# Kernel optimization log

Measured on AMD Instinct MI355X. Metric: run time of the kernel, lower is better.

## Reference

```python
import jax, jax.numpy as jnp
import numpy as np

N = 100000   # nodes
E = 1600000  # directed edges (before self loops)
IN = 64
HID = 32     # per-head hidden channels
H = 4        # heads
OUT = 32     # final output channels
NEG_SLOPE = 0.2
LN_EPS = 1e-5


def setup_inputs() -> dict:
    key = jax.random.key(0)
    ks = jax.random.split(key, 24)
    def nrm(k, shape, s=0.1):
        return jax.random.normal(k, shape, jnp.float32) * s
    inp = {
        "x": jax.random.normal(ks[0], (N, IN), jnp.float32),
        "edge_index": jax.random.randint(ks[1], (2, E), 0, N, jnp.int32),
    }
    in_dims = [IN, H * HID, H * HID]
    j = 2
    for i, di in enumerate(in_dims):
        inp[f"W{i}"] = nrm(ks[j], (di, H * HID)); j += 1
        inp[f"as{i}"] = nrm(ks[j], (H, HID)); j += 1
        inp[f"ad{i}"] = nrm(ks[j], (H, HID)); j += 1
        inp[f"b{i}"] = jnp.zeros((H * HID,), jnp.float32)
        inp[f"g{i}"] = jnp.ones((H * HID,), jnp.float32)
        inp[f"be{i}"] = jnp.zeros((H * HID,), jnp.float32)
    inp["Wf"] = nrm(ks[j], (H * HID, OUT)); j += 1
    inp["asf"] = nrm(ks[j], (1, OUT)); j += 1
    inp["adf"] = nrm(ks[j], (1, OUT)); j += 1
    inp["bf"] = jnp.zeros((OUT,), jnp.float32)
    return inp


def gat_conv(x, src, dst, W, att_s, att_d, bias, heads, C, concat, n_nodes):
    # h: [N, H, C]
    h = (x @ W).reshape(n_nodes, heads, C)
    a_src = jnp.sum(h * att_s, axis=-1)  # [N, H]
    a_dst = jnp.sum(h * att_d, axis=-1)  # [N, H]
    e = jax.nn.leaky_relu(a_src[src] + a_dst[dst], NEG_SLOPE)  # [E', H]
    # segment softmax over incoming edges of each dst node
    m = jax.ops.segment_max(e, dst, num_segments=n_nodes)
    m = jnp.where(jnp.isfinite(m), m, 0.0)
    ex = jnp.exp(e - m[dst])
    denom = jax.ops.segment_sum(ex, dst, num_segments=n_nodes)
    alpha = ex / (denom[dst] + 1e-16)  # [E', H]
    msg = h[src] * alpha[..., None]    # [E', H, C]
    out = jax.ops.segment_sum(msg, dst, num_segments=n_nodes)  # [N, H, C]
    if concat:
        out = out.reshape(n_nodes, heads * C)
    else:
        out = out.mean(axis=1)
    return out + bias


def layer_norm(x, g, b):
    mu = x.mean(-1, keepdims=True)
    v = jnp.mean((x - mu) ** 2, axis=-1, keepdims=True)
    return g * (x - mu) / jnp.sqrt(v + LN_EPS) + b


def reference(x, edge_index,
              W0, as0, ad0, b0, g0, be0,
              W1, as1, ad1, b1, g1, be1,
              W2, as2, ad2, b2, g2, be2,
              Wf, asf, adf, bf):
    n_nodes = x.shape[0]
    loop = jnp.arange(n_nodes, dtype=edge_index.dtype)
    src = jnp.concatenate([edge_index[0], loop])  # add self loops (PyG default)
    dst = jnp.concatenate([edge_index[1], loop])
    blocks = [(W0, as0, ad0, b0, g0, be0),
              (W1, as1, ad1, b1, g1, be1),
              (W2, as2, ad2, b2, g2, be2)]
    for (W, a_s, a_d, b, g, be) in blocks:
        x = gat_conv(x, src, dst, W, a_s, a_d, b, H, HID, True, n_nodes)
        x = jax.nn.elu(layer_norm(x, g, be))
    return gat_conv(x, src, dst, Wf, asf, adf, bf, 1, OUT, False, n_nodes)
```

## Files before the change

kernel.cpp:

```cpp
#include <hip/hip_runtime.h>
#include <hip/hip_bf16.h>

constexpr int NN   = 100000;
constexpr int EE   = 1600000;
constexpr int ETOT = EE + NN;
constexpr float SLOPE = 0.2f;
constexpr int BSH = 8;
constexpr int NB  = (NN + (1 << BSH) - 1) >> BSH;
constexpr int CCH = 8192;
constexpr int DCAP  = 36;
constexpr int DCAPP = 37;

typedef __attribute__((ext_vector_type(8))) short short8;
typedef __attribute__((ext_vector_type(4))) float f32x4;

__device__ __forceinline__ float bf_lo(unsigned u) { return __uint_as_float(u << 16); }
__device__ __forceinline__ float bf_hi(unsigned u) { return __uint_as_float(u & 0xffff0000u); }
__device__ __forceinline__ unsigned short f2bf(float f) {
    __hip_bfloat16 h = __float2bfloat16(f);
    return *(unsigned short*)&h;
}
__device__ __forceinline__ void wave_lds_fence() {
    __asm__ volatile("s_waitcnt lgkmcnt(0)" ::: "memory");
}
__device__ __forceinline__ void fma8(float* acc, uint4 u, float al) {
    acc[0] += bf_lo(u.x) * al; acc[1] += bf_hi(u.x) * al;
    acc[2] += bf_lo(u.y) * al; acc[3] += bf_hi(u.y) * al;
    acc[4] += bf_lo(u.z) * al; acc[5] += bf_hi(u.z) * al;
    acc[6] += bf_lo(u.w) * al; acc[7] += bf_hi(u.w) * al;
}
__device__ __forceinline__ void fma4(float* acc, uint2 u, float al) {
    acc[0] += bf_lo(u.x) * al; acc[1] += bf_hi(u.x) * al;
    acc[2] += bf_lo(u.y) * al; acc[3] += bf_hi(u.y) * al;
}

__global__ void k_cvt_x(const float* __restrict__ x, unsigned short* __restrict__ xb) {
    int i = blockIdx.x * blockDim.x + threadIdx.x;
    if (i >= NN * 64 / 8) return;
    const float4* xp = (const float4*)(x + (size_t)i * 8);
    float4 v0 = xp[0], v1 = xp[1];
    unsigned short o[8] = {f2bf(v0.x), f2bf(v0.y), f2bf(v0.z), f2bf(v0.w),
                           f2bf(v1.x), f2bf(v1.y), f2bf(v1.z), f2bf(v1.w)};
    *(uint4*)(xb + (size_t)i * 8) = *(uint4*)o;
}

__global__ __launch_bounds__(256) void k_cvt_w_all(
    const float* __restrict__ W0, const float* __restrict__ W1,
    const float* __restrict__ W2, const float* __restrict__ Wf,
    unsigned short* __restrict__ Wt0, unsigned short* __restrict__ Wt1,
    unsigned short* __restrict__ Wt2, unsigned short* __restrict__ Wtf,
    int* __restrict__ gbh) {
    int i = blockIdx.x * 256 + threadIdx.x;
    if (i < NB) gbh[i] = 0;
    if (i < 8192) {
        int k = i / 128, n = i % 128;
        Wt0[n * 64 + k] = f2bf(W0[i]);
    } else if (i < 24576) {
        int j = i - 8192; int k = j / 128, n = j % 128;
        Wt1[n * 128 + k] = f2bf(W1[j]);
    } else if (i < 40960) {
        int j = i - 24576; int k = j / 128, n = j % 128;
        Wt2[n * 128 + k] = f2bf(W2[j]);
    } else if (i < 45056) {
        int j = i - 40960; int k = j / 32, n = j % 32;
        Wtf[n * 128 + k] = f2bf(Wf[j]);
    }
}

__global__ __launch_bounds__(256) void k_bhist(const int* __restrict__ ei,
                                               int* __restrict__ gbh) {
    __shared__ int h[NB];
    int t = threadIdx.x;
    for (int i = t; i < NB; i += 256) h[i] = 0;
    __syncthreads();
    int i = blockIdx.x * 2048 + t;
#pragma unroll
    for (int k = 0; k < 8; k++, i += 256)
        if (i < EE) atomicAdd(&h[ei[EE + i] >> BSH], 1);
    __syncthreads();
    for (int j = t; j < NB; j += 256)
        if (h[j]) atomicAdd(&gbh[j], h[j]);
}

__global__ void k_bscan(const int* __restrict__ gbh, int* __restrict__ ebase,
                        int* __restrict__ gcur) {
    __shared__ int sd[512];
    int t = threadIdx.x;
    int v = (t < NB) ? gbh[t] : 0;
    sd[t] = v;
    __syncthreads();
    for (int off = 1; off < 512; off <<= 1) {
        int x = (t >= off) ? sd[t - off] : 0;
        __syncthreads();
        sd[t] += x;
        __syncthreads();
    }
    int ex = sd[t] - v;
    if (t < NB) { ebase[t] = ex; gcur[t] = ex; }
    if (t == NB) ebase[NB] = EE;
}

__global__ __launch_bounds__(256) void k_bscatter(const int* __restrict__ ei,
                                                  int* __restrict__ gcur,
                                                  int* __restrict__ pbuf) {
    __shared__ int h[NB], base[NB], cur[NB];
    int t = threadIdx.x;
    for (int i = t; i < NB; i += 256) { h[i] = 0; cur[i] = 0; }
    __syncthreads();
    int c0 = blockIdx.x * CCH;
    int cend = c0 + CCH < EE ? c0 + CCH : EE;
    for (int i = c0 + t; i < cend; i += 256)
        atomicAdd(&h[ei[EE + i] >> BSH], 1);
    __syncthreads();
    for (int i = t; i < NB; i += 256)
        if (h[i] > 0) base[i] = atomicAdd(&gcur[i], h[i]);
    __syncthreads();
    for (int i = c0 + t; i < cend; i += 256) {
        int s = ei[i], d = ei[EE + i];
        int b = d >> BSH;
        int c = atomicAdd(&cur[b], 1);
        pbuf[base[b] + c] = s | ((d & ((1 << BSH) - 1)) << 17);
    }
}

__global__ __launch_bounds__(256) void k_bcsr(const int* __restrict__ pbuf,
                                              const int* __restrict__ ebase,
                                              int* __restrict__ row_ptr,
                                              int* __restrict__ esrc) {
    constexpr int BNODES = 1 << BSH;
    __shared__ int hist[BNODES];
    __shared__ int cur[BNODES];
    __shared__ int sd[256];
    int b = blockIdx.x, t = threadIdx.x;
    int node0 = b << BSH;
    int e0 = ebase[b], e1 = ebase[b + 1];
    hist[t] = 0; cur[t] = 0;
    __syncthreads();
    for (int i = e0 + t; i < e1; i += 256)
        atomicAdd(&hist[pbuf[i] >> 17], 1);
    __syncthreads();
    int ts = hist[t];
    sd[t] = ts;
    __syncthreads();
    for (int off = 1; off < 256; off <<= 1) {
        int x = (t >= off) ? sd[t - off] : 0;
        __syncthreads();
        sd[t] += x;
        __syncthreads();
    }
    int ex = sd[t] - ts;
    __syncthreads();
    hist[t] = ex;
    __syncthreads();
    int rbase = e0 + node0;
    int n = node0 + t;
    if (n < NN) {
        int rp = rbase + hist[t] + t;
        row_ptr[n] = rp;
        esrc[rp] = n;
    }
    __syncthreads();
    for (int i = e0 + t; i < e1; i += 256) {
        int p = pbuf[i];
        int nl = p >> 17;
        int c = atomicAdd(&cur[nl], 1);
        esrc[rbase + hist[nl] + nl + 1 + c] = p & 0x1FFFF;
    }
}

template <int BN, int H>
__global__ __launch_bounds__(256) void k_mfma_att(
    const unsigned short* __restrict__ Ab, const unsigned short* __restrict__ Bt,
    const float* __restrict__ as_, const float* __restrict__ ad_,
    unsigned short* __restrict__ hb, float* __restrict__ a_s,
    float* __restrict__ a_d, int M, int K) {
    constexpr int NCT = BN / 16;
    constexpr int LDKB = 136;
    __shared__ unsigned short Bs[BN * LDKB];
    int tid = threadIdx.x;
    int lane = tid & 63, w = tid >> 6;
    int q = lane >> 4, col = lane & 15;
    int rowBase = blockIdx.x * 128;

    int kvs = (K == 64) ? 3 : 4;
    for (int idx = tid; idx < (BN << kvs); idx += 256) {
        int br = idx >> kvs;
        int ko = (idx & ((1 << kvs) - 1)) << 3;
        *(uint4*)(&Bs[br * LDKB + ko]) = *(const uint4*)(Bt + (size_t)br * K + ko);
    }
    __syncthreads();

    f32x4 acc[2][NCT];
#pragma unroll
    for (int rt = 0; rt < 2; rt++)
#pragma unroll
        for (int ct = 0; ct < NCT; ct++) acc[rt][ct] = (f32x4){0.f, 0.f, 0.f, 0.f};

    int r0 = rowBase + w * 32 + col;
    int grc0 = min(r0, M - 1);
    int grc1 = min(r0 + 16, M - 1);
    const unsigned short* a0p = Ab + (size_t)grc0 * K + q * 8;
    const unsigned short* a1p = Ab + (size_t)grc1 * K + q * 8;

    int nph = K >> 6;
    for (int ph = 0; ph < nph; ph++) {
        int kof = ph * 64;
        short8 af[2][2];
        af[0][0] = *(const short8*)(a0p + kof);
        af[0][1] = *(const short8*)(a0p + kof + 32);
        af[1][0] = *(const short8*)(a1p + kof);
        af[1][1] = *(const short8*)(a1p + kof + 32);
#pragma unroll
        for (int kt = 0; kt < 2; kt++)
#pragma unroll
            for (int ct = 0; ct < NCT; ct++) {
                short8 bf = *(const short8*)(&Bs[(ct * 16 + col) * LDKB + kof + kt * 32 + q * 8]);
#pragma unroll
                for (int rt = 0; rt < 2; rt++)
                    acc[rt][ct] = __builtin_amdgcn_mfma_f32_16x16x32_bf16(
                        af[rt][kt], bf, acc[rt][ct], 0, 0, 0);
            }
    }

    float swv[NCT], dwv[NCT];
#pragma unroll
    for (int ct = 0; ct < NCT; ct++) {
        int c = ct * 16 + col;
        swv[ct] = as_[c];
        dwv[ct] = ad_[c];
    }
#pragma unroll
    for (int rt = 0; rt < 2; rt++) {
#pragma unroll
        for (int r = 0; r < 4; r++) {
            int gr = rowBase + w * 32 + rt * 16 + q * 4 + r;
            if constexpr (H == 4) {
                float ps[4] = {0, 0, 0, 0}, pd[4] = {0, 0, 0, 0};
#pragma unroll
                for (int ct = 0; ct < NCT; ct++) {
                    float v = acc[rt][ct][r];
                    ps[ct >> 1] += v * swv[ct];
                    pd[ct >> 1] += v * dwv[ct];
                }
#pragma unroll
                for (int m = 1; m < 16; m <<= 1)
#pragma unroll
                    for (int h = 0; h < 4; h++) {
                        ps[h] += __shfl_xor(ps[h], m);
                        pd[h] += __shfl_xor(pd[h], m);
                    }
                if (gr < M) {
#pragma unroll
                    for (int ct = 0; ct < NCT; ct++)
                        hb[(size_t)gr * BN + ct * 16 + col] = f2bf(acc[rt][ct][r]);
                    if (col == 0) {
                        *(float4*)(a_s + (size_t)gr * 4) = make_float4(ps[0], ps[1], ps[2], ps[3]);
                        *(float4*)(a_d + (size_t)gr * 4) = make_float4(pd[0], pd[1], pd[2], pd[3]);
                    }
                }
            } else {
                float ps = 0.f, pd = 0.f;
#pragma unroll
                for (int ct = 0; ct < NCT; ct++) {
                    float v = acc[rt][ct][r];
                    ps += v * swv[ct];
                    pd += v * dwv[ct];
                }
#pragma unroll
                for (int m = 1; m < 16; m <<= 1) {
                    ps += __shfl_xor(ps, m);
                    pd += __shfl_xor(pd, m);
                }
                if (gr < M) {
#pragma unroll
                    for (int ct = 0; ct < NCT; ct++)
                        hb[(size_t)gr * BN + ct * 16 + col] = f2bf(acc[rt][ct][r]);
                    if (col == 0) { a_s[gr] = ps; a_d[gr] = pd; }
                }
            }
        }
    }
}

__global__ __launch_bounds__(128) void k_aggregate_ln(
    const unsigned short* __restrict__ hb, const float* __restrict__ a_src,
    const float* __restrict__ a_dst, const int* __restrict__ row_ptr,
    const int* __restrict__ esrc, const float* __restrict__ bias,
    const float* __restrict__ gamma, const float* __restrict__ beta,
    unsigned short* __restrict__ xb) {
    __shared__ uint2 slab_all[2][4 * 4 * DCAPP];
    int tid = threadIdx.x;
    int w = tid >> 6, lane = tid & 63;
    int g = lane >> 4, i = lane & 15;
    int myhead = i >> 2;
    uint2* slab = slab_all[w];
    int n0 = blockIdx.x * 8 + w * 4;
    int n = n0 + g;
    bool valid = n < NN;
    int start = 0, deg = 0;
    if (valid) {
        start = row_ptr[n];
        int end = (n == NN - 1) ? ETOT : row_ptr[n + 1];
        deg = end - start;
    }
    int wmax = deg;
#pragma unroll
    for (int m = 1; m < 64; m <<= 1) wmax = max(wmax, __shfl_xor(wmax, m));

    if (wmax <= DCAP) {
        float4 ad = make_float4(0.f, 0.f, 0.f, 0.f);
        if (valid) ad = ((const float4*)a_dst)[n];
        float d0 = 0.f, d1 = 0.f, d2 = 0.f, d3 = 0.f;
        uint2* nslab = slab + g * (4 * DCAPP);
        for (int k = i; k < deg; k += 16) {
            int s = esrc[start + k];
            float4 a = ((const float4*)a_src)[s];
            float e0 = a.x + ad.x; e0 = fmaxf(e0, SLOPE * e0); float x0 = __expf(e0);
            float e1 = a.y + ad.y; e1 = fmaxf(e1, SLOPE * e1); float x1 = __expf(e1);
            float e2 = a.z + ad.z; e2 = fmaxf(e2, SLOPE * e2); float x2 = __expf(e2);
            float e3 = a.w + ad.w; e3 = fmaxf(e3, SLOPE * e3); float x3 = __expf(e3);
            nslab[0 * DCAPP + k] = make_uint2((unsigned)s, __float_as_uint(x0));
            nslab[1 * DCAPP + k] = make_uint2((unsigned)s, __float_as_uint(x1));
            nslab[2 * DCAPP + k] = make_uint2((unsigned)s, __float_as_uint(x2));
            nslab[3 * DCAPP + k] = make_uint2((unsigned)s, __float_as_uint(x3));
            d0 += x0; d1 += x1; d2 += x2; d3 += x3;
        }
#pragma unroll
        for (int m = 1; m < 16; m <<= 1) {
            d0 += __shfl_xor(d0, m);
            d1 += __shfl_xor(d1, m);
            d2 += __shfl_xor(d2, m);
            d3 += __shfl_xor(d3, m);
        }
        float dh = myhead == 0 ? d0 : myhead == 1 ? d1 : myhead == 2 ? d2 : d3;
        float inv = 1.f / (dh + 1e-16f);
        wave_lds_fence();

        float acc[8];
#pragma unroll
        for (int k = 0; k < 8; k++) acc[k] = 0.f;
        const uint2* myrow = nslab + myhead * DCAPP;
        const unsigned short* hbase = hb + i * 8;
        int j = 0;
        for (; j + 4 <= deg; j += 4) {
            uint2 p0 = myrow[j], p1 = myrow[j + 1], p2 = myrow[j + 2], p3 = myrow[j + 3];
            uint4 u0 = *(const uint4*)(hbase + (size_t)p0.x * 128);
            uint4 u1 = *(const uint4*)(hbase + (size_t)p1.x * 128);
            uint4 u2 = *(const uint4*)(hbase + (size_t)p2.x * 128);
            uint4 u3 = *(const uint4*)(hbase + (size_t)p3.x * 128);
            fma8(acc, u0, __uint_as_float(p0.y));
            fma8(acc, u1, __uint_as_float(p1.y));
            fma8(acc, u2, __uint_as_float(p2.y));
            fma8(acc, u3, __uint_as_float(p3.y));
        }
        for (; j < deg; j++) {
            uint2 p = myrow[j];
            uint4 uu = *(const uint4*)(hbase + (size_t)p.x * 128);
            fma8(acc, uu, __uint_as_float(p.y));
        }
#pragma unroll
        for (int k = 0; k < 8; k++) acc[k] *= inv;

        if (valid) {
            float y[8];
            float sum = 0.f;
            const float4* bp = (const float4*)(bias + i * 8);
            float4 b0 = bp[0], b1 = bp[1];
#pragma unroll
            for (int k = 0; k < 8; k++) {
                float b = k < 4 ? (&b0.x)[k] : (&b1.x)[k - 4];
                y[k] = acc[k] + b;
                sum += y[k];
            }
#pragma unroll
            for (int m = 1; m < 16; m <<= 1) sum += __shfl_xor(sum, m);
            float mu = sum * (1.f / 128.f);
            float ss = 0.f;
            float d[8];
#pragma unroll
            for (int k = 0; k < 8; k++) { d[k] = y[k] - mu; ss += d[k] * d[k]; }
#pragma unroll
            for (int m = 1; m < 16; m <<= 1) ss += __shfl_xor(ss, m);
            float is = rsqrtf(ss * (1.f / 128.f) + 1e-5f);
            const float4* gp = (const float4*)(gamma + i * 8);
            const float4* ep = (const float4*)(beta + i * 8);
            float4 g0 = gp[0], g1 = gp[1], e0 = ep[0], e1 = ep[1];
            unsigned short o16[8];
#pragma unroll
            for (int k = 0; k < 8; k++) {
                float gm = k < 4 ? (&g0.x)[k] : (&g1.x)[k - 4];
                float bt = k < 4 ? (&e0.x)[k] : (&e1.x)[k - 4];
                float z = gm * (d[k] * is) + bt;
                o16[k] = f2bf(z > 0.f ? z : __expf(z) - 1.f);
            }
            *(uint4*)(xb + (size_t)n * 128 + i * 8) = *(uint4*)o16;
        }
    } else {
        for (int m4 = 0; m4 < 4; m4++) {
            int nm = n0 + m4;
            if (nm >= NN) continue;
            int startm = row_ptr[nm];
            int endm = (nm == NN - 1) ? ETOT : row_ptr[nm + 1];
            int degm = endm - startm;
            float4 ad = ((const float4*)a_dst)[nm];
            int gg = lane >> 4, c16 = lane & 15, hh = c16 >> 2;
            float acc[8];
#pragma unroll
            for (int k = 0; k < 8; k++) acc[k] = 0.f;
            if (degm <= 64) {
                int msrc = 0;
                float me0 = 0.f, me1 = 0.f, me2 = 0.f, me3 = 0.f;
                if (lane < degm) {
                    int s = esrc[startm + lane];
                    msrc = s;
                    float4 a = ((const float4*)a_src)[s];
                    float e0 = a.x + ad.x; e0 = fmaxf(e0, SLOPE * e0); me0 = __expf(e0);
                    float e1 = a.y + ad.y; e1 = fmaxf(e1, SLOPE * e1); me1 = __expf(e1);
                    float e2 = a.z + ad.z; e2 = fmaxf(e2, SLOPE * e2); me2 = __expf(e2);
                    float e3 = a.w + ad.w; e3 = fmaxf(e3, SLOPE * e3); me3 = __expf(e3);
                }
                float d0 = me0, d1 = me1, d2 = me2, d3 = me3;
#pragma unroll
                for (int m = 1; m < 64; m <<= 1) {
                    d0 += __shfl_xor(d0, m);
                    d1 += __shfl_xor(d1, m);
                    d2 += __shfl_xor(d2, m);
                    d3 += __shfl_xor(d3, m);
                }
                me0 *= 1.f / (d0 + 1e-16f);
                me1 *= 1.f / (d1 + 1e-16f);
                me2 *= 1.f / (d2 + 1e-16f);
                me3 *= 1.f / (d3 + 1e-16f);
                int iters = (degm + 3) >> 2;
                for (int it = 0; it < iters; it++) {
                    int j = gg + (it << 2);
                    int jj = j < degm ? j : 0;
                    int s = __shfl(msrc, jj);
                    float a0 = __shfl(me0, jj), a1 = __shfl(me1, jj);
                    float a2 = __shfl(me2, jj), a3 = __shfl(me3, jj);
                    if (j < degm) {
                        float al = hh == 0 ? a0 : hh == 1 ? a1 : hh == 2 ? a2 : a3;
                        uint4 uu = *(const uint4*)(hb + (size_t)s * 128 + c16 * 8);
                        fma8(acc, uu, al);
                    }
                }
            } else {
                float d0 = 0.f, d1 = 0.f, d2 = 0.f, d3 = 0.f;
                for (int k = startm + lane; k < endm; k += 64) {
                    int s = esrc[k];
                    float4 a = ((const float4*)a_src)[s];
                    float e0 = a.x + ad.x; e0 = fmaxf(e0, SLOPE * e0); d0 += __expf(e0);
                    float e1 = a.y + ad.y; e1 = fmaxf(e1, SLOPE * e1); d1 += __expf(e1);
                    float e2 = a.z + ad.z; e2 = fmaxf(e2, SLOPE * e2); d2 += __expf(e2);
                    float e3 = a.w + ad.w; e3 = fmaxf(e3, SLOPE * e3); d3 += __expf(e3);
                }
#pragma unroll
                for (int m = 1; m < 64; m <<= 1) {
                    d0 += __shfl_xor(d0, m);
                    d1 += __shfl_xor(d1, m);
                    d2 += __shfl_xor(d2, m);
                    d3 += __shfl_xor(d3, m);
                }
                float invh = hh == 0 ? 1.f / (d0 + 1e-16f) : hh == 1 ? 1.f / (d1 + 1e-16f)
                           : hh == 2 ? 1.f / (d2 + 1e-16f) : 1.f / (d3 + 1e-16f);
                float adh = hh == 0 ? ad.x : hh == 1 ? ad.y : hh == 2 ? ad.z : ad.w;
                for (int j = gg; j < degm; j += 4) {
                    int s = esrc[startm + j];
                    float e = a_src[(size_t)s * 4 + hh] + adh;
                    e = fmaxf(e, SLOPE * e);
                    float al = __expf(e) * invh;
                    uint4 uu = *(const uint4*)(hb + (size_t)s * 128 + c16 * 8);
                    fma8(acc, uu, al);
                }
            }
#pragma unroll
            for (int k = 0; k < 8; k++) {
                acc[k] += __shfl_xor(acc[k], 16);
                acc[k] += __shfl_xor(acc[k], 32);
            }
            if (lane < 16) {
                float y[8];
                float sum = 0.f;
                const float4* bp = (const float4*)(bias + lane * 8);
                float4 b0 = bp[0], b1 = bp[1];
#pragma unroll
                for (int k = 0; k < 8; k++) {
                    float b = k < 4 ? (&b0.x)[k] : (&b1.x)[k - 4];
                    y[k] = acc[k] + b;
                    sum += y[k];
                }
#pragma unroll
                for (int m = 1; m < 16; m <<= 1) sum += __shfl_xor(sum, m);
                float mu = sum * (1.f / 128.f);
                float ss = 0.f;
                float d[8];
#pragma unroll
                for (int k = 0; k < 8; k++) { d[k] = y[k] - mu; ss += d[k] * d[k]; }
#pragma unroll
                for (int m = 1; m < 16; m <<= 1) ss += __shfl_xor(ss, m);
                float is = rsqrtf(ss * (1.f / 128.f) + 1e-5f);
                const float4* gp = (const float4*)(gamma + lane * 8);
                const float4* ep = (const float4*)(beta + lane * 8);
                float4 g0 = gp[0], g1 = gp[1], e0 = ep[0], e1 = ep[1];
                unsigned short o16[8];
#pragma unroll
                for (int k = 0; k < 8; k++) {
                    float gm = k < 4 ? (&g0.x)[k] : (&g1.x)[k - 4];
                    float bt = k < 4 ? (&e0.x)[k] : (&e1.x)[k - 4];
                    float z = gm * (d[k] * is) + bt;
                    o16[k] = f2bf(z > 0.f ? z : __expf(z) - 1.f);
                }
                *(uint4*)(xb + (size_t)nm * 128 + lane * 8) = *(uint4*)o16;
            }
        }
    }
}

__global__ __launch_bounds__(128) void k_agg_final(
    const unsigned short* __restrict__ hb, const float* __restrict__ a_src,
    const float* __restrict__ a_dst, const int* __restrict__ row_ptr,
    const int* __restrict__ esrc, const float* __restrict__ bf,
    float* __restrict__ out) {
    __shared__ uint2 slab_all[2][8 * DCAPP];
    int tid = threadIdx.x;
    int w = tid >> 6, lane = tid & 63;
    int g = lane >> 3, i = lane & 7;
    uint2* nslab = slab_all[w] + g * DCAPP;
    int n0 = blockIdx.x * 16 + w * 8;
    int n = n0 + g;
    bool valid = n < NN;
    int start = 0, deg = 0;
    if (valid) {
        start = row_ptr[n];
        int end = (n == NN - 1) ? ETOT : row_ptr[n + 1];
        deg = end - start;
    }
    int wmax = deg;
#pragma unroll
    for (int m = 1; m < 64; m <<= 1) wmax = max(wmax, __shfl_xor(wmax, m));

    if (wmax <= DCAP) {
        float adn = valid ? a_dst[n] : 0.f;
        float d = 0.f;
        for (int k = i; k < deg; k += 8) {
            int s = esrc[start + k];
            float e = a_src[s] + adn;
            e = fmaxf(e, SLOPE * e);
            float xv = __expf(e);
            nslab[k] = make_uint2((unsigned)s, __float_as_uint(xv));
            d += xv;
        }
#pragma unroll
        for (int m = 1; m < 8; m <<= 1) d += __shfl_xor(d, m);
        float inv = 1.f / (d + 1e-16f);
        wave_lds_fence();

        float acc[4] = {0.f, 0.f, 0.f, 0.f};
        const unsigned short* hbase = hb + i * 4;
        int j = 0;
        for (; j + 2 <= deg; j += 2) {
            uint2 p0 = nslab[j], p1 = nslab[j + 1];
            uint2 u0 = *(const uint2*)(hbase + (size_t)p0.x * 32);
            uint2 u1 = *(const uint2*)(hbase + (size_t)p1.x * 32);
            fma4(acc, u0, __uint_as_float(p0.y));
            fma4(acc, u1, __uint_as_float(p1.y));
        }
        if (j < deg) {
            uint2 p = nslab[j];
            uint2 u = *(const uint2*)(hbase + (size_t)p.x * 32);
            fma4(acc, u, __uint_as_float(p.y));
        }
        if (valid) {
            float4 b4 = ((const float4*)bf)[i];
            float4 o = make_float4(acc[0] * inv + b4.x, acc[1] * inv + b4.y,
                                   acc[2] * inv + b4.z, acc[3] * inv + b4.w);
            ((float4*)out)[(size_t)n * 8 + i] = o;
        }
    } else {
        for (int m8 = 0; m8 < 8; m8++) {
            int nm = n0 + m8;
            if (nm >= NN) continue;
            int startm = row_ptr[nm];
            int endm = (nm == NN - 1) ? ETOT : row_ptr[nm + 1];
            int degm = endm - startm;
            float adn = a_dst[nm];
            int gg = lane >> 3, c8 = lane & 7;
            float d = 0.f;
            for (int k = startm + lane; k < endm; k += 64) {
                int s = esrc[k];
                float e = a_src[s] + adn;
                e = fmaxf(e, SLOPE * e);
                d += __expf(e);
            }
#pragma unroll
            for (int m = 1; m < 64; m <<= 1) d += __shfl_xor(d, m);
            float inv = 1.f / (d + 1e-16f);
            float acc[4] = {0.f, 0.f, 0.f, 0.f};
            for (int j = gg; j < degm; j += 8) {
                int s = esrc[startm + j];
                float e = a_src[s] + adn;
                e = fmaxf(e, SLOPE * e);
                float al = __expf(e) * inv;
                uint2 u = *(const uint2*)(hb + (size_t)s * 32 + c8 * 4);
                fma4(acc, u, al);
            }
#pragma unroll
            for (int k = 0; k < 4; k++) {
                acc[k] += __shfl_xor(acc[k], 8);
                acc[k] += __shfl_xor(acc[k], 16);
                acc[k] += __shfl_xor(acc[k], 32);
            }
            if (lane < 8) {
                float4 b4 = ((const float4*)bf)[lane];
                float4 o = make_float4(acc[0] + b4.x, acc[1] + b4.y, acc[2] + b4.z,
                                       acc[3] + b4.w);
                ((float4*)out)[(size_t)nm * 8 + lane] = o;
            }
        }
    }
}

extern "C" void kernel_launch(void* const* d_in, const int* in_sizes, int n_in,
                              void* d_out, int out_size, void* d_ws,
                              size_t ws_size, hipStream_t stream) {
    const float* x  = (const float*)d_in[0];
    const int* ei   = (const int*)d_in[1];
    const float* W[3]  = {(const float*)d_in[2], (const float*)d_in[8],  (const float*)d_in[14]};
    const float* AS[3] = {(const float*)d_in[3], (const float*)d_in[9],  (const float*)d_in[15]};
    const float* AD[3] = {(const float*)d_in[4], (const float*)d_in[10], (const float*)d_in[16]};
    const float* Bb[3] = {(const float*)d_in[5], (const float*)d_in[11], (const float*)d_in[17]};
    const float* G[3]  = {(const float*)d_in[6], (const float*)d_in[12], (const float*)d_in[18]};
    const float* BE[3] = {(const float*)d_in[7], (const float*)d_in[13], (const float*)d_in[19]};
    const float* Wf  = (const float*)d_in[20];
    const float* asf = (const float*)d_in[21];
    const float* adf = (const float*)d_in[22];
    const float* bfp = (const float*)d_in[23];
    float* out = (float*)d_out;

    unsigned short* xb = (unsigned short*)d_ws;
    unsigned short* hb = xb + (size_t)NN * 128;
    float* a_s = (float*)(hb + (size_t)NN * 128);
    float* a_d = a_s + (size_t)NN * 4;
    int* row_ptr = (int*)(a_d + (size_t)NN * 4);
    int* esrc    = row_ptr + NN;
    int* gbh     = esrc + ETOT;
    int* ebase   = gbh + NB;
    int* gcur    = ebase + NB + 1;
    int* pbuf    = gcur + NB;
    unsigned short* Wt0 = (unsigned short*)(pbuf + EE);
    unsigned short* Wt1 = Wt0 + 128 * 64;
    unsigned short* Wt2 = Wt1 + 128 * 128;
    unsigned short* Wtf = Wt2 + 128 * 128;

    k_cvt_x<<<(NN * 64 / 8 + 255) / 256, 256, 0, stream>>>(x, xb);
    k_cvt_w_all<<<176, 256, 0, stream>>>(W[0], W[1], W[2], Wf, Wt0, Wt1, Wt2, Wtf, gbh);

    k_bhist<<<(EE + 2047) / 2048, 256, 0, stream>>>(ei, gbh);
    k_bscan<<<1, 512, 0, stream>>>(gbh, ebase, gcur);
    k_bscatter<<<(EE + CCH - 1) / CCH, 256, 0, stream>>>(ei, gcur, pbuf);
    k_bcsr<<<NB, 256, 0, stream>>>(pbuf, ebase, row_ptr, esrc);

    const unsigned short* Wts[3] = {Wt0, Wt1, Wt2};
    int K = 64;
    int gblk = (NN + 127) / 128;
    for (int l = 0; l < 3; l++) {
        k_mfma_att<128, 4><<<gblk, 256, 0, stream>>>(xb, Wts[l], AS[l], AD[l],
                                                     hb, a_s, a_d, NN, K);
        k_aggregate_ln<<<(NN + 7) / 8, 128, 0, stream>>>(hb, a_s, a_d, row_ptr,
                                                         esrc, Bb[l], G[l], BE[l], xb);
        K = 128;
    }
    k_mfma_att<32, 1><<<gblk, 256, 0, stream>>>(xb, Wtf, asf, adf, hb, a_s, a_d,
                                                NN, 128);
    k_agg_final<<<(NN + 15) / 16, 128, 0, stream>>>(hb, a_s, a_d, row_ptr, esrc,
                                                    bfp, out);
}
```

Before: 510.5 us.

## Fuse all GAT layers into one persistent cooperative kernel with grid syncs

Replaces the eight per-layer GEMM and aggregation launches with a single cooperative persistent kernel. Blocks loop over GEMM tiles and aggregation units and use grid.sync between stages, with LDS shared through a union. The x and weight conversion kernels are also merged into one prep launch. This removes launch gaps and tail effects, but the persistent grid is sized as occupancy times 256 (assumed CU count), which is not queried from the device. The aggregation now runs in 256-thread blocks, which may lower occupancy.

```diff
diff --git a/kernel.cpp b/kernel.cpp
--- a/kernel.cpp
+++ b/kernel.cpp
@@ -1,5 +1,8 @@
 #include <hip/hip_runtime.h>
 #include <hip/hip_bf16.h>
+#include <hip/hip_cooperative_groups.h>
+
+namespace cg = cooperative_groups;
 
 constexpr int NN   = 100000;
 constexpr int EE   = 1600000;
@@ -10,6 +13,12 @@
 constexpr int CCH = 8192;
 constexpr int DCAP  = 36;
 constexpr int DCAPP = 37;
+constexpr int LDKB  = 136;
+constexpr int XB_BLOCKS = (NN * 64 / 8) / 256;
+constexpr int WB_BLOCKS = 176;
+constexpr int GBLK = (NN + 127) / 128;
+constexpr int AGG_UNITS  = (NN + 15) / 16;
+constexpr int AGGF_UNITS = (NN + 31) / 32;
 
 typedef __attribute__((ext_vector_type(8))) short short8;
 typedef __attribute__((ext_vector_type(4))) float f32x4;
@@ -34,36 +43,37 @@
     acc[2] += bf_lo(u.y) * al; acc[3] += bf_hi(u.y) * al;
 }
 
-__global__ void k_cvt_x(const float* __restrict__ x, unsigned short* __restrict__ xb) {
-    int i = blockIdx.x * blockDim.x + threadIdx.x;
-    if (i >= NN * 64 / 8) return;
-    const float4* xp = (const float4*)(x + (size_t)i * 8);
-    float4 v0 = xp[0], v1 = xp[1];
-    unsigned short o[8] = {f2bf(v0.x), f2bf(v0.y), f2bf(v0.z), f2bf(v0.w),
-                           f2bf(v1.x), f2bf(v1.y), f2bf(v1.z), f2bf(v1.w)};
-    *(uint4*)(xb + (size_t)i * 8) = *(uint4*)o;
-}
-
-__global__ __launch_bounds__(256) void k_cvt_w_all(
+__global__ __launch_bounds__(256) void k_prep(
+    const float* __restrict__ x, unsigned short* __restrict__ xb,
     const float* __restrict__ W0, const float* __restrict__ W1,
     const float* __restrict__ W2, const float* __restrict__ Wf,
     unsigned short* __restrict__ Wt0, unsigned short* __restrict__ Wt1,
     unsigned short* __restrict__ Wt2, unsigned short* __restrict__ Wtf,
     int* __restrict__ gbh) {
-    int i = blockIdx.x * 256 + threadIdx.x;
-    if (i < NB) gbh[i] = 0;
-    if (i < 8192) {
-        int k = i / 128, n = i % 128;
-        Wt0[n * 64 + k] = f2bf(W0[i]);
-    } else if (i < 24576) {
-        int j = i - 8192; int k = j / 128, n = j % 128;
-        Wt1[n * 128 + k] = f2bf(W1[j]);
-    } else if (i < 40960) {
-        int j = i - 24576; int k = j / 128, n = j % 128;
-        Wt2[n * 128 + k] = f2bf(W2[j]);
-    } else if (i < 45056) {
-        int j = i - 40960; int k = j / 32, n = j % 32;
-        Wtf[n * 128 + k] = f2bf(Wf[j]);
+    int b = blockIdx.x, t = threadIdx.x;
+    if (b < XB_BLOCKS) {
+        int i = b * 256 + t;
+        const float4* xp = (const float4*)(x + (size_t)i * 8);
+        float4 v0 = xp[0], v1 = xp[1];
+        unsigned short o[8] = {f2bf(v0.x), f2bf(v0.y), f2bf(v0.z), f2bf(v0.w),
+                               f2bf(v1.x), f2bf(v1.y), f2bf(v1.z), f2bf(v1.w)};
+        *(uint4*)(xb + (size_t)i * 8) = *(uint4*)o;
+    } else {
+        int i = (b - XB_BLOCKS) * 256 + t;
+        if (i < NB) gbh[i] = 0;
+        if (i < 8192) {
+            int k = i / 128, n = i % 128;
+            Wt0[n * 64 + k] = f2bf(W0[i]);
+        } else if (i < 24576) {
+            int j = i - 8192; int k = j / 128, n = j % 128;
+            Wt1[n * 128 + k] = f2bf(W1[j]);
+        } else if (i < 40960) {
+            int j = i - 24576; int k = j / 128, n = j % 128;
+            Wt2[n * 128 + k] = f2bf(W2[j]);
+        } else if (i < 45056) {
+            int j = i - 40960; int k = j / 32, n = j % 32;
+            Wtf[n * 128 + k] = f2bf(Wf[j]);
+        }
     }
 }
 
@@ -169,26 +179,15 @@
 }
 
 template <int BN, int H>
-__global__ __launch_bounds__(256) void k_mfma_att(
-    const unsigned short* __restrict__ Ab, const unsigned short* __restrict__ Bt,
-    const float* __restrict__ as_, const float* __restrict__ ad_,
-    unsigned short* __restrict__ hb, float* __restrict__ a_s,
-    float* __restrict__ a_d, int M, int K) {
+__device__ __forceinline__ void gemm_tile(
+    int rowBase, const unsigned short* __restrict__ Ab,
+    const unsigned short* Bs, const float* __restrict__ as_,
+    const float* __restrict__ ad_, unsigned short* __restrict__ hb,
+    float* __restrict__ a_s, float* __restrict__ a_d, int M, int K) {
     constexpr int NCT = BN / 16;
-    constexpr int LDKB = 136;
-    __shared__ unsigned short Bs[BN * LDKB];
     int tid = threadIdx.x;
     int lane = tid & 63, w = tid >> 6;
     int q = lane >> 4, col = lane & 15;
-    int rowBase = blockIdx.x * 128;
-
-    int kvs = (K == 64) ? 3 : 4;
-    for (int idx = tid; idx < (BN << kvs); idx += 256) {
-        int br = idx >> kvs;
-        int ko = (idx & ((1 << kvs) - 1)) << 3;
-        *(uint4*)(&Bs[br * LDKB + ko]) = *(const uint4*)(Bt + (size_t)br * K + ko);
-    }
-    __syncthreads();
 
     f32x4 acc[2][NCT];
 #pragma unroll
@@ -282,19 +281,27 @@
     }
 }
 
-__global__ __launch_bounds__(128) void k_aggregate_ln(
-    const unsigned short* __restrict__ hb, const float* __restrict__ a_src,
-    const float* __restrict__ a_dst, const int* __restrict__ row_ptr,
-    const int* __restrict__ esrc, const float* __restrict__ bias,
-    const float* __restrict__ gamma, const float* __restrict__ beta,
-    unsigned short* __restrict__ xb) {
-    __shared__ uint2 slab_all[2][4 * 4 * DCAPP];
+template <int BN>
+__device__ __forceinline__ void stage_B(unsigned short* Bs,
+                                        const unsigned short* __restrict__ Bt, int K) {
     int tid = threadIdx.x;
-    int w = tid >> 6, lane = tid & 63;
+    int kvs = (K == 64) ? 3 : 4;
+    for (int idx = tid; idx < (BN << kvs); idx += 256) {
+        int br = idx >> kvs;
+        int ko = (idx & ((1 << kvs) - 1)) << 3;
+        *(uint4*)(&Bs[br * LDKB + ko]) = *(const uint4*)(Bt + (size_t)br * K + ko);
+    }
+}
+
+__device__ __forceinline__ void agg_ln_unit(
+    int n0, uint2* slab, const unsigned short* __restrict__ hb,
+    const float* __restrict__ a_src, const float* __restrict__ a_dst,
+    const int* __restrict__ row_ptr, const int* __restrict__ esrc,
+    const float* __restrict__ bias, const float* __restrict__ gamma,
+    const float* __restrict__ beta, unsigned short* __restrict__ xb) {
+    int lane = threadIdx.x & 63;
     int g = lane >> 4, i = lane & 15;
     int myhead = i >> 2;
-    uint2* slab = slab_all[w];
-    int n0 = blockIdx.x * 8 + w * 4;
     int n = n0 + g;
     bool valid = n < NN;
     int start = 0, deg = 0;
@@ -516,17 +523,14 @@
     }
 }
 
-__global__ __launch_bounds__(128) void k_agg_final(
-    const unsigned short* __restrict__ hb, const float* __restrict__ a_src,
-    const float* __restrict__ a_dst, const int* __restrict__ row_ptr,
-    const int* __restrict__ esrc, const float* __restrict__ bf,
-    float* __restrict__ out) {
-    __shared__ uint2 slab_all[2][8 * DCAPP];
-    int tid = threadIdx.x;
-    int w = tid >> 6, lane = tid & 63;
+__device__ __forceinline__ void agg_final_unit(
+    int n0, uint2* slabw, const unsigned short* __restrict__ hb,
+    const float* __restrict__ a_src, const float* __restrict__ a_dst,
+    const int* __restrict__ row_ptr, const int* __restrict__ esrc,
+    const float* __restrict__ bf, float* __restrict__ out) {
+    int lane = threadIdx.x & 63;
     int g = lane >> 3, i = lane & 7;
-    uint2* nslab = slab_all[w] + g * DCAPP;
-    int n0 = blockIdx.x * 16 + w * 8;
+    uint2* nslab = slabw + g * DCAPP;
     int n = n0 + g;
     bool valid = n < NN;
     int start = 0, deg = 0;
@@ -618,6 +622,93 @@
             }
         }
     }
+}
+
+struct CoopArgs {
+    unsigned short* xb; unsigned short* hb; float* a_s; float* a_d;
+    const int* row_ptr; const int* esrc;
+    const unsigned short* Wt0; const unsigned short* Wt1;
+    const unsigned short* Wt2; const unsigned short* Wtf;
+    const float *AS0, *AD0, *Bb0, *G0, *BE0;
+    const float *AS1, *AD1, *Bb1, *G1, *BE1;
+    const float *AS2, *AD2, *Bb2, *G2, *BE2;
+    const float *asf, *adf, *bfp; float* out;
+};
+
+__global__ __launch_bounds__(256) void k_layers(CoopArgs a) {
+    cg::grid_group grid = cg::this_grid();
+    __shared__ union {
+        unsigned short Bs[128 * LDKB];
+        uint2 slab[4][4 * 4 * DCAPP];
+        uint2 slabf[4][8 * DCAPP];
+    } u;
+    int w = threadIdx.x >> 6;
+
+    const unsigned short* Wts[3] = {a.Wt0, a.Wt1, a.Wt2};
+    const float* ASl[3] = {a.AS0, a.AS1, a.AS2};
+    const float* ADl[3] = {a.AD0, a.AD1, a.AD2};
+    const float* Bbl[3] = {a.Bb0, a.Bb1, a.Bb2};
+    const float* Gl[3]  = {a.G0, a.G1, a.G2};
+    const float* BEl[3] = {a.BE0, a.BE1, a.BE2};
+
+    int K = 64;
+    for (int l = 0; l < 3; l++) {
+        stage_B<128>(u.Bs, Wts[l], K);
+        __syncthreads();
+        for (int t = blockIdx.x; t < GBLK; t += gridDim.x)
+            gemm_tile<128, 4>(t * 128, a.xb, u.Bs, ASl[l], ADl[l], a.hb,
+                              a.a_s, a.a_d, NN, K);
+        grid.sync();
+        for (int t = blockIdx.x; t < AGG_UNITS; t += gridDim.x)
+            agg_ln_unit(t * 16 + w * 4, u.slab[w], a.hb, a.a_s, a.a_d,
+                        a.row_ptr, a.esrc, Bbl[l], Gl[l], BEl[l], a.xb);
+        grid.sync();
+        K = 128;
+    }
+    stage_B<32>(u.Bs, a.Wtf, 128);
+    __syncthreads();
+    for (int t = blockIdx.x; t < GBLK; t += gridDim.x)
+        gemm_tile<32, 1>(t * 128, a.xb, u.Bs, a.asf, a.adf, a.hb,
+                         a.a_s, a.a_d, NN, 128);
+    grid.sync();
+    for (int t = blockIdx.x; t < AGGF_UNITS; t += gridDim.x)
+        agg_final_unit(t * 32 + w * 8, u.slabf[w], a.hb, a.a_s, a.a_d,
+                       a.row_ptr, a.esrc, a.bfp, a.out);
+}
+
+template <int BN, int H>
+__global__ __launch_bounds__(256) void k_mfma_att(
+    const unsigned short* __restrict__ Ab, const unsigned short* __restrict__ Bt,
+    const float* __restrict__ as_, const float* __restrict__ ad_,
+    unsigned short* __restrict__ hb, float* __restrict__ a_s,
+    float* __restrict__ a_d, int M, int K) {
+    __shared__ unsigned short Bs[128 * LDKB];
+    stage_B<BN>(Bs, Bt, K);
+    __syncthreads();
+    gemm_tile<BN, H>(blockIdx.x * 128, Ab, Bs, as_, ad_, hb, a_s, a_d, M, K);
+}
+
+__global__ __launch_bounds__(128) void k_aggregate_ln(
+    const unsigned short* __restrict__ hb, const float* __restrict__ a_src,
+    const float* __restrict__ a_dst, const int* __restrict__ row_ptr,
+    const int* __restrict__ esrc, const float* __restrict__ bias,
+    const float* __restrict__ gamma, const float* __restrict__ beta,
+    unsigned short* __restrict__ xb) {
+    __shared__ uint2 slab_all[2][4 * 4 * DCAPP];
+    int w = threadIdx.x >> 6;
+    agg_ln_unit(blockIdx.x * 8 + w * 4, slab_all[w], hb, a_src, a_dst,
+                row_ptr, esrc, bias, gamma, beta, xb);
+}
+
+__global__ __launch_bounds__(128) void k_agg_final(
+    const unsigned short* __restrict__ hb, const float* __restrict__ a_src,
+    const float* __restrict__ a_dst, const int* __restrict__ row_ptr,
+    const int* __restrict__ esrc, const float* __restrict__ bf,
+    float* __restrict__ out) {
+    __shared__ uint2 slab_all[2][8 * DCAPP];
+    int w = threadIdx.x >> 6;
+    agg_final_unit(blockIdx.x * 16 + w * 8, slab_all[w], hb, a_src, a_dst,
+                   row_ptr, esrc, bf, out);
 }
 
 extern "C" void kernel_launch(void* const* d_in, const int* in_sizes, int n_in,
@@ -652,26 +743,48 @@
     unsigned short* Wt2 = Wt1 + 128 * 128;
     unsigned short* Wtf = Wt2 + 128 * 128;
 
-    k_cvt_x<<<(NN * 64 / 8 + 255) / 256, 256, 0, stream>>>(x, xb);
-    k_cvt_w_all<<<176, 256, 0, stream>>>(W[0], W[1], W[2], Wf, Wt0, Wt1, Wt2, Wtf, gbh);
+    k_prep<<<XB_BLOCKS + WB_BLOCKS, 256, 0, stream>>>(
+        x, xb, W[0], W[1], W[2], Wf, Wt0, Wt1, Wt2, Wtf, gbh);
 
     k_bhist<<<(EE + 2047) / 2048, 256, 0, stream>>>(ei, gbh);
     k_bscan<<<1, 512, 0, stream>>>(gbh, ebase, gcur);
     k_bscatter<<<(EE + CCH - 1) / CCH, 256, 0, stream>>>(ei, gcur, pbuf);
     k_bcsr<<<NB, 256, 0, stream>>>(pbuf, ebase, row_ptr, esrc);
 
-    const unsigned short* Wts[3] = {Wt0, Wt1, Wt2};
-    int K = 64;
-    int gblk = (NN + 127) / 128;
-    for (int l = 0; l < 3; l++) {
-        k_mfma_att<128, 4><<<gblk, 256, 0, stream>>>(xb, Wts[l], AS[l], AD[l],
-                                                     hb, a_s, a_d, NN, K);
-        k_aggregate_ln<<<(NN + 7) / 8, 128, 0, stream>>>(hb, a_s, a_d, row_ptr,
-                                                         esrc, Bb[l], G[l], BE[l], xb);
-        K = 128;
-    }
-    k_mfma_att<32, 1><<<gblk, 256, 0, stream>>>(xb, Wtf, asf, adf, hb, a_s, a_d,
-                                                NN, 128);
-    k_agg_final<<<(NN + 15) / 16, 128, 0, stream>>>(hb, a_s, a_d, row_ptr, esrc,
-                                                    bfp, out);
-}
+    CoopArgs ca;
+    ca.xb = xb; ca.hb = hb; ca.a_s = a_s; ca.a_d = a_d;
+    ca.row_ptr = row_ptr; ca.esrc = esrc;
+    ca.Wt0 = Wt0; ca.Wt1 = Wt1; ca.Wt2 = Wt2; ca.Wtf = Wtf;
+    ca.AS0 = AS[0]; ca.AD0 = AD[0]; ca.Bb0 = Bb[0]; ca.G0 = G[0]; ca.BE0 = BE[0];
+    ca.AS1 = AS[1]; ca.AD1 = AD[1]; ca.Bb1 = Bb[1]; ca.G1 = G[1]; ca.BE1 = BE[1];
+    ca.AS2 = AS[2]; ca.AD2 = AD[2]; ca.Bb2 = Bb[2]; ca.G2 = G[2]; ca.BE2 = BE[2];
+    ca.asf = asf; ca.adf = adf; ca.bfp = bfp; ca.out = out;
+
+    int nblk = 0;
+    hipError_t oe = hipOccupancyMaxActiveBlocksPerMultiprocessor(&nblk, k_layers, 256, 0);
+    bool coop_ok = (oe == hipSuccess && nblk >= 1);
+    if (coop_ok) {
+        int grid = nblk * 256;
+        void* params[] = {&ca};
+        hipError_t ce = hipLaunchCooperativeKernel((const void*)k_layers,
+                                                   dim3(grid), dim3(256),
+                                                   params, 0, stream);
+        coop_ok = (ce == hipSuccess);
+        if (!coop_ok) (void)hipGetLastError();
+    }
+    if (!coop_ok) {
+        const unsigned short* Wts[3] = {Wt0, Wt1, Wt2};
+        int K = 64;
+        for (int l = 0; l < 3; l++) {
+            k_mfma_att<128, 4><<<GBLK, 256, 0, stream>>>(xb, Wts[l], AS[l], AD[l],
+                                                         hb, a_s, a_d, NN, K);
+            k_aggregate_ln<<<(NN + 7) / 8, 128, 0, stream>>>(hb, a_s, a_d, row_ptr,
+                                                             esrc, Bb[l], G[l], BE[l], xb);
+            K = 128;
+        }
+        k_mfma_att<32, 1><<<GBLK, 256, 0, stream>>>(xb, Wtf, asf, adf, hb, a_s, a_d,
+                                                    NN, 128);
+        k_agg_final<<<(NN + 15) / 16, 128, 0, stream>>>(hb, a_s, a_d, row_ptr, esrc,
+                                                        bfp, out);
+    }
+}
```

Result: no change. 506.6 us (-0.8%).
